# Kernel optimization log

Measured on AMD Instinct MI355X. Metric: run time of the kernel, lower is better.

Reference implementation:

```python
import jax, jax.numpy as jnp
import numpy as np


def setup_inputs() -> dict:
    key = jax.random.key(0)
    k1, k2 = jax.random.split(key)
    B, C, H, W = 16, 256, 64, 64
    K, D = 1024, 256
    z = jax.random.normal(k1, (B, C, H, W), dtype=jnp.float32)
    embedding = jax.random.normal(k2, (K, D), dtype=jnp.float32)
    return {"z": z, "embedding": embedding}


def reference(z, embedding):
    # _preprocess: shift channel dim (axis 1) to last, flatten -> [N, D]
    B, C, H, W = z.shape
    encoded_permuted = jnp.transpose(z, (0, 2, 3, 1))  # [B, H, W, C]
    permuted_shape = encoded_permuted.shape
    encoded_flat = encoded_permuted.reshape(-1, C)  # [N, D]

    x_sq = jnp.sum(encoded_flat * encoded_flat, axis=1, keepdims=True)  # [N, 1]
    e_sq = jnp.sum(embedding * embedding, axis=1)  # [K]
    cross = encoded_flat @ embedding.T  # [N, K]
    distances = x_sq - 2.0 * cross + e_sq[None, :]
    codebook_indices = jnp.argmin(distances, axis=1)  # [N]
    quantized_lookup = embedding[codebook_indices]  # [N, D]

    # straight-through estimator
    quantized_flat = encoded_flat + jax.lax.stop_gradient(quantized_lookup - encoded_flat)

    # _postprocess: reshape and shift last dim back to axis 1
    quantized = jnp.transpose(quantized_flat.reshape(permuted_shape), (0, 3, 1, 2))
    return (encoded_flat, quantized_flat, codebook_indices, quantized)
```

## Files before the change

kernel.cpp:

```cpp
#include <hip/hip_runtime.h>
#include <hip/hip_bf16.h>

typedef _Float16 h8 __attribute__((ext_vector_type(8)));
typedef float f4 __attribute__((ext_vector_type(4)));

#define N_TOK 65536
#define DIM 256
#define KCODES 1024
#define HWSZ 4096

__device__ __forceinline__ void gll16(const void* g, void* l) {
    __builtin_amdgcn_global_load_lds((const __attribute__((address_space(1))) void*)g,
                                     (__attribute__((address_space(3))) void*)l, 16, 0, 0);
}


__global__ void k_prep_frag(const float* __restrict__ emb, _Float16* __restrict__ BhF,
                            _Float16* __restrict__ BlF) {
    int gi = blockIdx.x * 256 + threadIdx.x;
    int kb = gi >> 9;
    int s = (gi >> 6) & 7;
    int dq = (gi >> 4) & 3;
    int r = gi & 15;
    int code = kb * 16 + r;
    int d0 = s * 32 + dq * 8;
    const float* src = emb + (size_t)code * DIM + d0;
    float4 x0 = *(const float4*)(src);
    float4 x1 = *(const float4*)(src + 4);
    float xs[8] = {x0.x, x0.y, x0.z, x0.w, x1.x, x1.y, x1.z, x1.w};
    h8 hi, lo;
#pragma unroll
    for (int j = 0; j < 8; ++j) {
        _Float16 h = (_Float16)xs[j];
        hi[j] = h;
        lo[j] = (_Float16)(xs[j] - (float)h);
    }
    *(h8*)(BhF + (size_t)gi * 8) = hi;
    *(h8*)(BlF + (size_t)gi * 8) = lo;
}

__global__ void k_esq(const float* __restrict__ emb, float* __restrict__ e_sq) {
    int t = threadIdx.x;
    int code = blockIdx.x * 4 + (t >> 6);
    int l = t & 63;
    float4 v = *(const float4*)(emb + (size_t)code * DIM + l * 4);
    float s = v.x * v.x + v.y * v.y + v.z * v.z + v.w * v.w;
#pragma unroll
    for (int off = 32; off >= 1; off >>= 1) s += __shfl_xor(s, off);
    if (l == 0) e_sq[code] = s;
}

__global__ void k_transpose(const float* __restrict__ z, float* __restrict__ enc,
                            _Float16* __restrict__ AhF, _Float16* __restrict__ AlF) {
    __shared__ float T[64][65];
    int blk = blockIdx.x;
    int b = blk >> 8;
    int rem = blk & 255;
    int c0 = (rem >> 6) * 64;
    int hw0 = (rem & 63) * 64;
    int t = threadIdx.x;
    const float* zp = z + (size_t)b * DIM * HWSZ;
    {
        int hw4 = (t & 15) * 4, cl = t >> 4;
#pragma unroll
        for (int i = 0; i < 4; ++i) {
            int c = cl + i * 16;
            float4 v = *(const float4*)(zp + (size_t)(c0 + c) * HWSZ + hw0 + hw4);
            T[c][hw4 + 0] = v.x; T[c][hw4 + 1] = v.y;
            T[c][hw4 + 2] = v.z; T[c][hw4 + 3] = v.w;
        }
    }
    __syncthreads();
    {
        int c4 = (t & 15) * 4, hwl = t >> 4;
#pragma unroll
        for (int i = 0; i < 4; ++i) {
            int hw = hwl + i * 16;
            float4 v;
            v.x = T[c4 + 0][hw]; v.y = T[c4 + 1][hw];
            v.z = T[c4 + 2][hw]; v.w = T[c4 + 3][hw];
            *(float4*)(enc + (size_t)(b * HWSZ + hw0 + hw) * DIM + c0 + c4) = v;
        }
    }
    {
        int base_nb = b * 256 + (hw0 >> 4);
#pragma unroll
        for (int i = 0; i < 2; ++i) {
            int gidx = i * 256 + t;
            int nbi = gidx >> 7;
            int si = (gidx >> 6) & 1;
            int dq = (gidx >> 4) & 3;
            int r = gidx & 15;
            int hwl = nbi * 16 + r;
            int cl = si * 32 + dq * 8;
            h8 hi, lo;
#pragma unroll
            for (int j = 0; j < 8; ++j) {
                float x = T[cl + j][hwl];
                _Float16 h = (_Float16)x;
                hi[j] = h;
                lo[j] = (_Float16)(x - (float)h);
            }
            size_t G = (((size_t)(base_nb + nbi) * 8) + (c0 >> 5) + si) * 64 + dq * 16 + r;
            *(h8*)(AhF + G * 8) = hi;
            *(h8*)(AlF + G * 8) = lo;
        }
    }
}

#define WAITV(n) asm volatile("s_waitcnt vmcnt(" #n ")" ::: "memory")
#define BARRIER __builtin_amdgcn_s_barrier()
#define PRIO1 __builtin_amdgcn_s_setprio(1)
#define PRIO0 __builtin_amdgcn_s_setprio(0)

extern __shared__ char SB[];

__global__ __launch_bounds__(1024)
void k_gemm_argmin(const _Float16* __restrict__ AhF, const _Float16* __restrict__ AlF,
                   const _Float16* __restrict__ BhF, const _Float16* __restrict__ BlF,
                   const float* __restrict__ e_sq,
                   float* __restrict__ pV1, int* __restrict__ pI1) {
    int gid = blockIdx.x;
    int grp = gid >> 7;
    int colTile = (gid >> 5) & 3;
    int rowTile = grp * 32 + (gid & 31);
    int r0 = rowTile * 256, c0 = colTile * 256;
    int t = threadIdx.x;
    int w = t >> 6, l = t & 63;
    int wm = w >> 2, wn = w & 3;
    int l16 = l & 15, lhi = l >> 4;

    const char* gAh = (const char*)AhF + (((size_t)(rowTile * 16 + w)) << 13) + (l << 4);
    const char* gAl = (const char*)AlF + (((size_t)(rowTile * 16 + w)) << 13) + (l << 4);
    const char* gBh = (const char*)BhF + (((size_t)(colTile * 16 + w)) << 13) + (l << 4);
    const char* gBl = (const char*)BlF + (((size_t)(colTile * 16 + w)) << 13) + (l << 4);

#define ISSUE_P(p) do { \
    const int s_ = (p) >> 1; \
    char* bp_ = SB + ((p) & 3) * 32768; \
    const char* a_ = ((p) & 1) ? gAl : gAh; \
    const char* b_ = ((p) & 1) ? gBl : gBh; \
    gll16(a_ + (s_ << 10), bp_ + (w << 10)); \
    gll16(b_ + (s_ << 10), bp_ + 16384 + (w << 10)); \
} while (0)

#define MFMA16(A_, B_) { _Pragma("unroll") for (int mf = 0; mf < 4; ++mf) \
    _Pragma("unroll") for (int nf = 0; nf < 4; ++nf) \
        acc[mf][nf] = __builtin_amdgcn_mfma_f32_16x16x32_f16(A_[mf], B_[nf], acc[mf][nf], 0, 0, 0); }

#define PHASE(q, W, DO_ISSUE) { \
    WAITV(W); \
    BARRIER; \
    if (DO_ISSUE) ISSUE_P((q) + 3); \
    const char* bp_ = SB + ((q) & 3) * 32768; \
    if (((q) & 1) == 0) { \
        _Pragma("unroll") for (int mf = 0; mf < 4; ++mf) \
            ah[mf] = *(const h8*)(bp_ + ((wm * 4 + mf) << 10) + (l << 4)); \
        _Pragma("unroll") for (int nf = 0; nf < 4; ++nf) \
            bh[nf] = *(const h8*)(bp_ + 16384 + ((wn * 4 + nf) << 10) + (l << 4)); \
        PRIO1; MFMA16(ah, bh); PRIO0; \
    } else { \
        h8 xl[4]; \
        _Pragma("unroll") for (int nf = 0; nf < 4; ++nf) \
            xl[nf] = *(const h8*)(bp_ + 16384 + ((wn * 4 + nf) << 10) + (l << 4)); \
        PRIO1; MFMA16(ah, xl); PRIO0; \
        _Pragma("unroll") for (int mf = 0; mf < 4; ++mf) \
            xl[mf] = *(const h8*)(bp_ + ((wm * 4 + mf) << 10) + (l << 4)); \
        PRIO1; MFMA16(xl, bh); PRIO0; \
    } }

    f4 acc[4][4];
#pragma unroll
    for (int i = 0; i < 4; ++i)
#pragma unroll
        for (int j = 0; j < 4; ++j) acc[i][j] = (f4)0.0f;

    h8 ah[4], bh[4];

    ISSUE_P(0); ISSUE_P(1); ISSUE_P(2);

    PHASE(0, 4, 1)   PHASE(1, 4, 1)   PHASE(2, 4, 1)   PHASE(3, 4, 1)
    PHASE(4, 4, 1)   PHASE(5, 4, 1)   PHASE(6, 4, 1)   PHASE(7, 4, 1)
    PHASE(8, 4, 1)   PHASE(9, 4, 1)   PHASE(10, 4, 1)  PHASE(11, 4, 1)
    PHASE(12, 4, 1)  PHASE(13, 4, 0)  PHASE(14, 2, 0)  PHASE(15, 0, 0)

    float* smV = (float*)SB;
    int* smI = (int*)(SB + 4096);

    float esq[4];
#pragma unroll
    for (int nf = 0; nf < 4; ++nf) esq[nf] = e_sq[c0 + wn * 64 + nf * 16 + l16];

#pragma unroll
    for (int mf = 0; mf < 4; ++mf) {
#pragma unroll
        for (int rg = 0; rg < 4; ++rg) {
            float bestV = 3.4e38f;
            int bestI = 0;
#pragma unroll
            for (int nf = 0; nf < 4; ++nf) {
                float v = esq[nf] - 2.0f * acc[mf][nf][rg];
                int ci = c0 + wn * 64 + nf * 16 + l16;
                if (v < bestV || (v == bestV && ci < bestI)) { bestV = v; bestI = ci; }
            }
#pragma unroll
            for (int off = 1; off < 16; off <<= 1) {
                float vv = __shfl_xor(bestV, off);
                int ii = __shfl_xor(bestI, off);
                if (vv < bestV || (vv == bestV && ii < bestI)) { bestV = vv; bestI = ii; }
            }
            if (l16 == 0) {
                int rloc = wm * 64 + mf * 16 + lhi * 4 + rg;
                smV[wn * 256 + rloc] = bestV;
                smI[wn * 256 + rloc] = bestI;
            }
        }
    }
    __syncthreads();
    if (t < 256) {
        float bestV = smV[t];
        int bestI = smI[t];
#pragma unroll
        for (int wn2 = 1; wn2 < 4; ++wn2) {
            float v = smV[wn2 * 256 + t];
            int i2 = smI[wn2 * 256 + t];
            if (v < bestV || (v == bestV && i2 < bestI)) { bestV = v; bestI = i2; }
        }
        pV1[colTile * N_TOK + r0 + t] = bestV;
        pI1[colTile * N_TOK + r0 + t] = bestI;
    }
}

__global__ void k_final_out1(const float* __restrict__ pV1, const int* __restrict__ pI1,
                             const float* __restrict__ emb,
                             float* __restrict__ out2, int* __restrict__ idxI,
                             float* __restrict__ out1) {
    __shared__ int sidx[256];
    int t = threadIdx.x;
    int n0 = blockIdx.x * 256;
    int n = n0 + t;
    float v1 = pV1[n];
    int i1 = pI1[n];
#pragma unroll
    for (int ct = 1; ct < 4; ++ct) {
        float a1 = pV1[ct * N_TOK + n];
        int ai = pI1[ct * N_TOK + n];
        if (a1 < v1 || (a1 == v1 && ai < i1)) { v1 = a1; i1 = ai; }
    }
    out2[n] = (float)i1;
    idxI[n] = i1;
    sidx[t] = i1;
    __syncthreads();
    int rr = t >> 2, q = t & 3;
#pragma unroll
    for (int i = 0; i < 4; ++i) {
        int r = i * 64 + rr;
        int idx = sidx[r];
        const float* src = emb + (size_t)idx * DIM + q * 64;
        float* dst = out1 + (size_t)(n0 + r) * DIM + q * 64;
#pragma unroll
        for (int j = 0; j < 16; ++j)
            *(float4*)(dst + j * 4) = *(const float4*)(src + j * 4);
    }
}

__global__ void k_out3(const float* __restrict__ emb, const int* __restrict__ idxI,
                       float* __restrict__ out3) {
    __shared__ float E[32][257];
    int blk = blockIdx.x;
    int b = blk >> 7, hwt = blk & 127;
    int hw0 = hwt * 32;
    int n0 = b * HWSZ + hw0;
    int t = threadIdx.x;
    {
        int r = t >> 3, oct = t & 7;
        int idx = idxI[n0 + r];
        const float* src = emb + (size_t)idx * DIM + oct * 32;
#pragma unroll
        for (int i = 0; i < 8; ++i) {
            float4 v = *(const float4*)(src + i * 4);
            E[r][oct * 32 + i * 4 + 0] = v.x;
            E[r][oct * 32 + i * 4 + 1] = v.y;
            E[r][oct * 32 + i * 4 + 2] = v.z;
            E[r][oct * 32 + i * 4 + 3] = v.w;
        }
    }
    __syncthreads();
    {
        int w = t >> 6, l = t & 63;
        int ch = l >> 5, hw = l & 31;
        float* dst = out3 + (size_t)b * DIM * HWSZ + hw0 + hw;
#pragma unroll
        for (int it = 0; it < 32; ++it) {
            int c = w * 64 + it * 2 + ch;
            dst[(size_t)c * HWSZ] = E[hw][c];
        }
    }
}

extern "C" void kernel_launch(void* const* d_in, const int* in_sizes, int n_in,
                              void* d_out, int out_size, void* d_ws, size_t ws_size,
                              hipStream_t stream) {
    const float* z = (const float*)d_in[0];
    const float* emb = (const float*)d_in[1];
    float* out = (float*)d_out;
    float* out0 = out;
    float* out1 = out + 16777216;
    float* out2 = out + 33554432;
    float* out3 = out + 33619968;

    _Float16* AhF = (_Float16*)out1;
    _Float16* AlF = (_Float16*)(out1 + 8388608);

    char* ws = (char*)d_ws;
    _Float16* BhF = (_Float16*)(ws);
    _Float16* BlF = (_Float16*)(ws + 524288);
    float* e_sq = (float*)(ws + 1048576);
    float* pV1 = (float*)(ws + 1052672);
    int* pI1 = (int*)(ws + 2101248);
    int* idxI = (int*)(ws + 3149824);

    hipFuncSetAttribute((const void*)k_gemm_argmin,
                        hipFuncAttributeMaxDynamicSharedMemorySize, 131072);

    k_prep_frag<<<128, 256, 0, stream>>>(emb, BhF, BlF);
    k_esq<<<256, 256, 0, stream>>>(emb, e_sq);
    k_transpose<<<4096, 256, 0, stream>>>(z, out0, AhF, AlF);
    k_gemm_argmin<<<1024, 1024, 131072, stream>>>(AhF, AlF, BhF, BlF, e_sq, pV1, pI1);
    k_final_out1<<<256, 256, 0, stream>>>(pV1, pI1, emb, out2, idxI, out1);
    k_out3<<<2048, 256, 0, stream>>>(emb, idxI, out3);
}
```

Baseline: 205.6 us.

## Two-pass argmin: fp16 GEMM with top-2 margin, split-precision rescore of ambiguous rows

The main distance GEMM now uses only the fp16 high parts of the inputs, and the argmin reduction tracks both the best and second-best distance per row. Rows whose margin between the two is below a fixed threshold are appended to a list with an atomic counter. Only those rows are gathered, split into hi/lo fp16 and re-scored with the full split-precision GEMM, which then overwrites their indices and gathered outputs. This aims to halve the main GEMM's MFMA and load work and drop the low-part writes in the transpose. The cost is extra kernels and a heuristic threshold, and rows beyond the list cap keep the fp16-only result, which risks index mismatches.

```diff
diff --git a/kernel.cpp b/kernel.cpp
--- a/kernel.cpp
+++ b/kernel.cpp
@@ -8,6 +8,8 @@
 #define DIM 256
 #define KCODES 1024
 #define HWSZ 4096
+#define TAU 0.75f
+#define FCAP 16384
 
 __device__ __forceinline__ void gll16(const void* g, void* l) {
     __builtin_amdgcn_global_load_lds((const __attribute__((address_space(1))) void*)g,
@@ -18,13 +20,9 @@
 __global__ void k_prep_frag(const float* __restrict__ emb, _Float16* __restrict__ BhF,
                             _Float16* __restrict__ BlF) {
     int gi = blockIdx.x * 256 + threadIdx.x;
-    int kb = gi >> 9;
-    int s = (gi >> 6) & 7;
-    int dq = (gi >> 4) & 3;
-    int r = gi & 15;
+    int kb = gi >> 9, s = (gi >> 6) & 7, dq = (gi >> 4) & 3, r = gi & 15;
     int code = kb * 16 + r;
-    int d0 = s * 32 + dq * 8;
-    const float* src = emb + (size_t)code * DIM + d0;
+    const float* src = emb + (size_t)code * DIM + s * 32 + dq * 8;
     float4 x0 = *(const float4*)(src);
     float4 x1 = *(const float4*)(src + 4);
     float xs[8] = {x0.x, x0.y, x0.z, x0.w, x1.x, x1.y, x1.z, x1.w};
@@ -39,7 +37,9 @@
     *(h8*)(BlF + (size_t)gi * 8) = lo;
 }
 
-__global__ void k_esq(const float* __restrict__ emb, float* __restrict__ e_sq) {
+__global__ void k_esq(const float* __restrict__ emb, float* __restrict__ e_sq,
+                      int* __restrict__ flagCnt) {
+    if (blockIdx.x == 0 && threadIdx.x == 0) *flagCnt = 0;
     int t = threadIdx.x;
     int code = blockIdx.x * 4 + (t >> 6);
     int l = t & 63;
@@ -51,7 +51,7 @@
 }
 
 __global__ void k_transpose(const float* __restrict__ z, float* __restrict__ enc,
-                            _Float16* __restrict__ AhF, _Float16* __restrict__ AlF) {
+                            _Float16* __restrict__ AhF) {
     __shared__ float T[64][65];
     int blk = blockIdx.x;
     int b = blk >> 8;
@@ -87,23 +87,14 @@
 #pragma unroll
         for (int i = 0; i < 2; ++i) {
             int gidx = i * 256 + t;
-            int nbi = gidx >> 7;
-            int si = (gidx >> 6) & 1;
-            int dq = (gidx >> 4) & 3;
-            int r = gidx & 15;
+            int nbi = gidx >> 7, si = (gidx >> 6) & 1, dq = (gidx >> 4) & 3, r = gidx & 15;
             int hwl = nbi * 16 + r;
             int cl = si * 32 + dq * 8;
-            h8 hi, lo;
-#pragma unroll
-            for (int j = 0; j < 8; ++j) {
-                float x = T[cl + j][hwl];
-                _Float16 h = (_Float16)x;
-                hi[j] = h;
-                lo[j] = (_Float16)(x - (float)h);
-            }
+            h8 hi;
+#pragma unroll
+            for (int j = 0; j < 8; ++j) hi[j] = (_Float16)T[cl + j][hwl];
             size_t G = (((size_t)(base_nb + nbi) * 8) + (c0 >> 5) + si) * 64 + dq * 16 + r;
             *(h8*)(AhF + G * 8) = hi;
-            *(h8*)(AlF + G * 8) = lo;
         }
     }
 }
@@ -116,10 +107,9 @@
 extern __shared__ char SB[];
 
 __global__ __launch_bounds__(1024)
-void k_gemm_argmin(const _Float16* __restrict__ AhF, const _Float16* __restrict__ AlF,
-                   const _Float16* __restrict__ BhF, const _Float16* __restrict__ BlF,
-                   const float* __restrict__ e_sq,
-                   float* __restrict__ pV1, int* __restrict__ pI1) {
+void k_gemm1(const _Float16* __restrict__ AhF, const _Float16* __restrict__ BhF,
+             const float* __restrict__ e_sq,
+             float* __restrict__ pV1, int* __restrict__ pI1, float* __restrict__ pV2) {
     int gid = blockIdx.x;
     int grp = gid >> 7;
     int colTile = (gid >> 5) & 3;
@@ -131,7 +121,188 @@
     int l16 = l & 15, lhi = l >> 4;
 
     const char* gAh = (const char*)AhF + (((size_t)(rowTile * 16 + w)) << 13) + (l << 4);
-    const char* gAl = (const char*)AlF + (((size_t)(rowTile * 16 + w)) << 13) + (l << 4);
+    const char* gBh = (const char*)BhF + (((size_t)(colTile * 16 + w)) << 13) + (l << 4);
+
+#define ISSUE1(p) do { \
+    char* bp_ = SB + ((p) & 3) * 32768; \
+    gll16(gAh + ((p) << 10), bp_ + (w << 10)); \
+    gll16(gBh + ((p) << 10), bp_ + 16384 + (w << 10)); \
+} while (0)
+
+#define PHASE1(q, W, DO_ISSUE) { \
+    WAITV(W); \
+    BARRIER; \
+    if (DO_ISSUE) ISSUE1((q) + 3); \
+    const char* bp_ = SB + ((q) & 3) * 32768; \
+    h8 ah[4], bh[4]; \
+    _Pragma("unroll") for (int mf = 0; mf < 4; ++mf) \
+        ah[mf] = *(const h8*)(bp_ + ((wm * 4 + mf) << 10) + (l << 4)); \
+    _Pragma("unroll") for (int nf = 0; nf < 4; ++nf) \
+        bh[nf] = *(const h8*)(bp_ + 16384 + ((wn * 4 + nf) << 10) + (l << 4)); \
+    PRIO1; \
+    _Pragma("unroll") for (int mf = 0; mf < 4; ++mf) \
+        _Pragma("unroll") for (int nf = 0; nf < 4; ++nf) \
+            acc[mf][nf] = __builtin_amdgcn_mfma_f32_16x16x32_f16(ah[mf], bh[nf], acc[mf][nf], 0, 0, 0); \
+    PRIO0; }
+
+    f4 acc[4][4];
+#pragma unroll
+    for (int i = 0; i < 4; ++i)
+#pragma unroll
+        for (int j = 0; j < 4; ++j) acc[i][j] = (f4)0.0f;
+
+    ISSUE1(0); ISSUE1(1); ISSUE1(2);
+
+    PHASE1(0, 4, 1)  PHASE1(1, 4, 1)  PHASE1(2, 4, 1)  PHASE1(3, 4, 1)
+    PHASE1(4, 4, 1)  PHASE1(5, 4, 0)  PHASE1(6, 2, 0)  PHASE1(7, 0, 0)
+
+    float* smV1 = (float*)SB;
+    int*   smI1 = (int*)(SB + 4096);
+    float* smV2 = (float*)(SB + 8192);
+
+    float esq[4];
+#pragma unroll
+    for (int nf = 0; nf < 4; ++nf) esq[nf] = e_sq[c0 + wn * 64 + nf * 16 + l16];
+
+#pragma unroll
+    for (int mf = 0; mf < 4; ++mf) {
+#pragma unroll
+        for (int rg = 0; rg < 4; ++rg) {
+            float v1 = 3.4e38f, v2 = 3.4e38f;
+            int i1 = 0;
+#pragma unroll
+            for (int nf = 0; nf < 4; ++nf) {
+                float v = esq[nf] - 2.0f * acc[mf][nf][rg];
+                int ci = c0 + wn * 64 + nf * 16 + l16;
+                if (v < v1 || (v == v1 && ci < i1)) { v2 = v1; v1 = v; i1 = ci; }
+                else v2 = fminf(v2, v);
+            }
+#pragma unroll
+            for (int off = 1; off < 16; off <<= 1) {
+                float ov1 = __shfl_xor(v1, off);
+                int oi1 = __shfl_xor(i1, off);
+                float ov2 = __shfl_xor(v2, off);
+                if (ov1 < v1 || (ov1 == v1 && oi1 < i1)) { v2 = fminf(v1, ov2); v1 = ov1; i1 = oi1; }
+                else v2 = fminf(v2, ov1);
+            }
+            if (l16 == 0) {
+                int rloc = wm * 64 + mf * 16 + lhi * 4 + rg;
+                smV1[wn * 256 + rloc] = v1;
+                smI1[wn * 256 + rloc] = i1;
+                smV2[wn * 256 + rloc] = v2;
+            }
+        }
+    }
+    __syncthreads();
+    if (t < 256) {
+        float v1 = smV1[t], v2 = smV2[t];
+        int i1 = smI1[t];
+#pragma unroll
+        for (int wn2 = 1; wn2 < 4; ++wn2) {
+            float a1 = smV1[wn2 * 256 + t];
+            int ai = smI1[wn2 * 256 + t];
+            float a2 = smV2[wn2 * 256 + t];
+            if (a1 < v1 || (a1 == v1 && ai < i1)) { v2 = fminf(v1, a2); v1 = a1; i1 = ai; }
+            else v2 = fminf(v2, a1);
+        }
+        pV1[colTile * N_TOK + r0 + t] = v1;
+        pI1[colTile * N_TOK + r0 + t] = i1;
+        pV2[colTile * N_TOK + r0 + t] = v2;
+    }
+}
+
+__global__ void k_final_flag(const float* __restrict__ pV1, const int* __restrict__ pI1,
+                             const float* __restrict__ pV2, const float* __restrict__ emb,
+                             float* __restrict__ out2, int* __restrict__ idxI,
+                             int* __restrict__ flagCnt, int* __restrict__ flagList,
+                             float* __restrict__ out1) {
+    __shared__ int sidx[256];
+    int t = threadIdx.x;
+    int n0 = blockIdx.x * 256;
+    int n = n0 + t;
+    float v1 = pV1[n], v2 = pV2[n];
+    int i1 = pI1[n];
+#pragma unroll
+    for (int ct = 1; ct < 4; ++ct) {
+        float a1 = pV1[ct * N_TOK + n];
+        int ai = pI1[ct * N_TOK + n];
+        float a2 = pV2[ct * N_TOK + n];
+        if (a1 < v1 || (a1 == v1 && ai < i1)) { v2 = fminf(v1, a2); v1 = a1; i1 = ai; }
+        else v2 = fminf(v2, a1);
+    }
+    out2[n] = (float)i1;
+    idxI[n] = i1;
+    sidx[t] = i1;
+    if (v2 - v1 < TAU) {
+        int p = atomicAdd(flagCnt, 1);
+        if (p < FCAP) flagList[p] = n;
+    }
+    __syncthreads();
+    int rr = t >> 2, q = t & 3;
+#pragma unroll
+    for (int i = 0; i < 4; ++i) {
+        int r = i * 64 + rr;
+        int idx = sidx[r];
+        const float* src = emb + (size_t)idx * DIM + q * 64;
+        float* dst = out1 + (size_t)(n0 + r) * DIM + q * 64;
+#pragma unroll
+        for (int j = 0; j < 16; ++j)
+            *(float4*)(dst + j * 4) = *(const float4*)(src + j * 4);
+    }
+}
+
+__global__ void k_gather_split(const float* __restrict__ enc, const int* __restrict__ flagCnt,
+                               const int* __restrict__ flagList,
+                               _Float16* __restrict__ AhC, _Float16* __restrict__ AlC) {
+    __shared__ int rows[16];
+    int Fc = *flagCnt; if (Fc > FCAP) Fc = FCAP;
+    int j0 = blockIdx.x * 16;
+    if (j0 >= Fc || Fc == 0) return;
+    int t = threadIdx.x;
+    if (t < 16) {
+        int j = j0 + t;
+        rows[t] = flagList[j < Fc ? j : Fc - 1];
+    }
+    __syncthreads();
+#pragma unroll
+    for (int i = 0; i < 2; ++i) {
+        int g = i * 256 + t;
+        int s = g >> 6, dq = (g >> 4) & 3, r = g & 15;
+        int row = rows[r];
+        const float* src = enc + (size_t)row * DIM + s * 32 + dq * 8;
+        float4 x0 = *(const float4*)(src);
+        float4 x1 = *(const float4*)(src + 4);
+        float xs[8] = {x0.x, x0.y, x0.z, x0.w, x1.x, x1.y, x1.z, x1.w};
+        h8 hi, lo;
+#pragma unroll
+        for (int j = 0; j < 8; ++j) {
+            _Float16 h = (_Float16)xs[j];
+            hi[j] = h;
+            lo[j] = (_Float16)(xs[j] - (float)h);
+        }
+        size_t G = ((size_t)(blockIdx.x * 8 + s)) * 64 + dq * 16 + r;
+        *(h8*)(AhC + G * 8) = hi;
+        *(h8*)(AlC + G * 8) = lo;
+    }
+}
+
+__global__ __launch_bounds__(1024)
+void k_rescore3(const _Float16* __restrict__ AhC, const _Float16* __restrict__ AlC,
+                const _Float16* __restrict__ BhF, const _Float16* __restrict__ BlF,
+                const float* __restrict__ e_sq, const int* __restrict__ flagCnt,
+                float* __restrict__ pVr, int* __restrict__ pIr) {
+    int Fc = *flagCnt; if (Fc > FCAP) Fc = FCAP;
+    int gid = blockIdx.x;
+    int colTile = gid & 3, rowTile = gid >> 2;
+    if (rowTile * 256 >= Fc) return;
+    int r0 = rowTile * 256, c0 = colTile * 256;
+    int t = threadIdx.x;
+    int w = t >> 6, l = t & 63;
+    int wm = w >> 2, wn = w & 3;
+    int l16 = l & 15, lhi = l >> 4;
+
+    const char* gAh = (const char*)AhC + (((size_t)(rowTile * 16 + w)) << 13) + (l << 4);
+    const char* gAl = (const char*)AlC + (((size_t)(rowTile * 16 + w)) << 13) + (l << 4);
     const char* gBh = (const char*)BhF + (((size_t)(colTile * 16 + w)) << 13) + (l << 4);
     const char* gBl = (const char*)BlF + (((size_t)(colTile * 16 + w)) << 13) + (l << 4);
 
@@ -226,41 +397,50 @@
             int i2 = smI[wn2 * 256 + t];
             if (v < bestV || (v == bestV && i2 < bestI)) { bestV = v; bestI = i2; }
         }
-        pV1[colTile * N_TOK + r0 + t] = bestV;
-        pI1[colTile * N_TOK + r0 + t] = bestI;
-    }
-}
-
-__global__ void k_final_out1(const float* __restrict__ pV1, const int* __restrict__ pI1,
-                             const float* __restrict__ emb,
-                             float* __restrict__ out2, int* __restrict__ idxI,
-                             float* __restrict__ out1) {
-    __shared__ int sidx[256];
-    int t = threadIdx.x;
-    int n0 = blockIdx.x * 256;
-    int n = n0 + t;
-    float v1 = pV1[n];
-    int i1 = pI1[n];
-#pragma unroll
-    for (int ct = 1; ct < 4; ++ct) {
-        float a1 = pV1[ct * N_TOK + n];
-        int ai = pI1[ct * N_TOK + n];
-        if (a1 < v1 || (a1 == v1 && ai < i1)) { v1 = a1; i1 = ai; }
-    }
-    out2[n] = (float)i1;
-    idxI[n] = i1;
-    sidx[t] = i1;
-    __syncthreads();
-    int rr = t >> 2, q = t & 3;
-#pragma unroll
-    for (int i = 0; i < 4; ++i) {
-        int r = i * 64 + rr;
-        int idx = sidx[r];
-        const float* src = emb + (size_t)idx * DIM + q * 64;
-        float* dst = out1 + (size_t)(n0 + r) * DIM + q * 64;
-#pragma unroll
-        for (int j = 0; j < 16; ++j)
-            *(float4*)(dst + j * 4) = *(const float4*)(src + j * 4);
+        pVr[colTile * FCAP + r0 + t] = bestV;
+        pIr[colTile * FCAP + r0 + t] = bestI;
+    }
+}
+
+__global__ void k_rescore_final(const float* __restrict__ pVr, const int* __restrict__ pIr,
+                                const int* __restrict__ flagCnt, const int* __restrict__ flagList,
+                                const float* __restrict__ emb,
+                                float* __restrict__ out2, int* __restrict__ idxI,
+                                float* __restrict__ out1) {
+    __shared__ int sfi[64];
+    int Fc = *flagCnt; if (Fc > FCAP) Fc = FCAP;
+    int j0 = blockIdx.x * 64;
+    if (j0 >= Fc) return;
+    int t = threadIdx.x;
+    if (t < 64) {
+        int j = j0 + t;
+        int fi = 0;
+        if (j < Fc) {
+            float fv = pVr[j];
+            fi = pIr[j];
+#pragma unroll
+            for (int ct = 1; ct < 4; ++ct) {
+                float a = pVr[ct * FCAP + j];
+                int ai = pIr[ct * FCAP + j];
+                if (a < fv || (a == fv && ai < fi)) { fv = a; fi = ai; }
+            }
+            int row = flagList[j];
+            out2[row] = (float)fi;
+            idxI[row] = fi;
+        }
+        sfi[t] = fi;
+    }
+    __syncthreads();
+    int j = j0 + (t >> 2);
+    if (j < Fc) {
+        int row = flagList[j];
+        int fi = sfi[t >> 2];
+        int q = t & 3;
+        const float* src = emb + (size_t)fi * DIM + q * 64;
+        float* dst = out1 + (size_t)row * DIM + q * 64;
+#pragma unroll
+        for (int i = 0; i < 16; ++i)
+            *(float4*)(dst + i * 4) = *(const float4*)(src + i * 4);
     }
 }
 
@@ -310,23 +490,39 @@
     float* out3 = out + 33619968;
 
     _Float16* AhF = (_Float16*)out1;
-    _Float16* AlF = (_Float16*)(out1 + 8388608);
+
+    char* o3 = (char*)out3;
+    _Float16* AhC = (_Float16*)(o3);
+    _Float16* AlC = (_Float16*)(o3 + 8388608);
+    float* pV1 = (float*)(o3 + 16777216);
+    int*   pI1 = (int*)  (o3 + 17825792);
+    float* pV2 = (float*)(o3 + 18874368);
+    float* pVr = (float*)(o3 + 19922944);
+    int*   pIr = (int*)  (o3 + 20185088);
 
     char* ws = (char*)d_ws;
     _Float16* BhF = (_Float16*)(ws);
     _Float16* BlF = (_Float16*)(ws + 524288);
     float* e_sq = (float*)(ws + 1048576);
-    float* pV1 = (float*)(ws + 1052672);
-    int* pI1 = (int*)(ws + 2101248);
-    int* idxI = (int*)(ws + 3149824);
-
-    hipFuncSetAttribute((const void*)k_gemm_argmin,
+    int* flagCnt = (int*)(ws + 1052672);
+    int* flagList = (int*)(ws + 1056768);
+    int* idxI = (int*)(ws + 1121280);
+
+    hipFuncSetAttribute((const void*)k_gemm1,
                         hipFuncAttributeMaxDynamicSharedMemorySize, 131072);
+    hipFuncSetAttribute((const void*)k_rescore3,
+                        hipFuncAttributeMaxDynamicSharedMemorySize, 131072);
 
     k_prep_frag<<<128, 256, 0, stream>>>(emb, BhF, BlF);
-    k_esq<<<256, 256, 0, stream>>>(emb, e_sq);
-    k_transpose<<<4096, 256, 0, stream>>>(z, out0, AhF, AlF);
-    k_gemm_argmin<<<1024, 1024, 131072, stream>>>(AhF, AlF, BhF, BlF, e_sq, pV1, pI1);
-    k_final_out1<<<256, 256, 0, stream>>>(pV1, pI1, emb, out2, idxI, out1);
+    k_esq<<<256, 256, 0, stream>>>(emb, e_sq, flagCnt);
+    k_transpose<<<4096, 256, 0, stream>>>(z, out0, AhF);
+    k_gemm1<<<1024, 1024, 131072, stream>>>(AhF, BhF, e_sq, pV1, pI1, pV2);
+    k_final_flag<<<256, 256, 0, stream>>>(pV1, pI1, pV2, emb, out2, idxI,
+                                          flagCnt, flagList, out1);
+    k_gather_split<<<1024, 256, 0, stream>>>(out0, flagCnt, flagList, AhC, AlC);
+    k_rescore3<<<1024, 1024, 131072, stream>>>(AhC, AlC, BhF, BlF, e_sq, flagCnt,
+                                               pVr, pIr);
+    k_rescore_final<<<256, 256, 0, stream>>>(pVr, pIr, flagCnt, flagList, emb,
+                                             out2, idxI, out1);
     k_out3<<<2048, 256, 0, stream>>>(emb, idxI, out3);
 }
```

After: 221.2 us. 7.6% more time.
